# Kernel tuning notes

Measured on AMD Instinct MI355X. Metric: run time of the kernel, lower is better.

The kernel has to match this reference:

```python
import jax, jax.numpy as jnp
import numpy as np

N_NODES = 100000
N_HEDGES = 25000
N_EDGES = 1000000
NUM_GRAPHS = 64
H = 64


def _seg_mean(vals, idx, num_segments):
    s = jax.ops.segment_sum(vals, idx, num_segments=num_segments)
    cnt = jax.ops.segment_sum(jnp.ones((vals.shape[0],), vals.dtype), idx, num_segments=num_segments)
    return s / jnp.maximum(cnt, 1.0)[:, None]


def _sage(x_src, x_dst, src, dst, Wl, bl, Wr):
    # gather src features per edge, scatter-mean to dst, then lin_l(agg)+lin_r(x_dst)
    agg = _seg_mean(x_src[src], dst, x_dst.shape[0])
    return agg @ Wl + bl + x_dst @ Wr


def setup_inputs() -> dict:
    key = jax.random.key(0)
    ks = jax.random.split(key, 32)
    d = {}
    d['node_x'] = jax.random.normal(ks[0], (N_NODES, 1), jnp.float32)
    d['edge_x'] = jax.random.normal(ks[1], (N_HEDGES, 2), jnp.float32)
    d['n2e_src'] = jax.random.randint(ks[2], (N_EDGES,), 0, N_NODES)
    d['n2e_dst'] = jax.random.randint(ks[3], (N_EDGES,), 0, N_HEDGES)
    d['e2n_src'] = jax.random.randint(ks[4], (N_EDGES,), 0, N_HEDGES)
    d['e2n_dst'] = jax.random.randint(ks[5], (N_EDGES,), 0, N_NODES)
    d['node_batch'] = jnp.sort(jax.random.randint(ks[6], (N_NODES,), 0, NUM_GRAPHS))
    d['edge_batch'] = jnp.sort(jax.random.randint(ks[7], (N_HEDGES,), 0, NUM_GRAPHS))
    def w(k, shape, fan_in):
        return jax.random.normal(k, shape, jnp.float32) / np.sqrt(fan_in)
    d['Wn'] = w(ks[8], (1, H), 1); d['bn'] = jnp.zeros((H,), jnp.float32)
    d['We'] = w(ks[9], (2, H), 2); d['be'] = jnp.zeros((H,), jnp.float32)
    names = ['1l_n2e', '1r_n2e', '1l_e2n', '1r_e2n', '2l_n2e', '2r_n2e', '2l_e2n', '2r_e2n']
    for i, nm in enumerate(names):
        d['W' + nm] = w(ks[10 + i], (H, H), H)
        if 'l' in nm.split('_')[0]:
            d['b' + nm] = jnp.zeros((H,), jnp.float32)
    d['Wout'] = w(ks[20], (2 * H, 32), 2 * H)
    d['bout'] = jnp.zeros((32,), jnp.float32)
    return d


def reference(node_x, edge_x, n2e_src, n2e_dst, e2n_src, e2n_dst, node_batch, edge_batch,
              Wn, bn, We, be,
              W1l_n2e, b1l_n2e, W1r_n2e, W1l_e2n, b1l_e2n, W1r_e2n,
              W2l_n2e, b2l_n2e, W2r_n2e, W2l_e2n, b2l_e2n, W2r_e2n,
              Wout, bout):
    xn = jax.nn.relu(node_x @ Wn + bn)      # [N, H]
    xe = jax.nn.relu(edge_x @ We + be)      # [E_h, H]
    # HeteroConv layer 1 (each dst type has exactly one incoming edge type)
    xe1 = jax.nn.relu(_sage(xn, xe, n2e_src, n2e_dst, W1l_n2e, b1l_n2e, W1r_n2e))
    xn1 = jax.nn.relu(_sage(xe, xn, e2n_src, e2n_dst, W1l_e2n, b1l_e2n, W1r_e2n))
    # HeteroConv layer 2
    xe2 = jax.nn.relu(_sage(xn1, xe1, n2e_src, n2e_dst, W2l_n2e, b2l_n2e, W2r_n2e))
    xn2 = jax.nn.relu(_sage(xe1, xn1, e2n_src, e2n_dst, W2l_e2n, b2l_e2n, W2r_e2n))
    node_pool = _seg_mean(xn2, node_batch, NUM_GRAPHS)  # [G, H]
    edge_pool = _seg_mean(xe2, edge_batch, NUM_GRAPHS)  # [G, H]
    combined = jnp.concatenate([node_pool, edge_pool], axis=-1)  # [G, 2H]
    return combined @ Wout + bout  # [G, 32]
```

## Files before the change

### kernel.cpp

```cpp
#include <hip/hip_runtime.h>

#define N_NODES 100000
#define N_HEDGES 25000
#define N_EDGES 1000000
#define NG 64
#define HD 64

#define EB_SH 8
#define EB_NB 98
#define EB_CAP 12000
#define NB_SH 9
#define NB_NB 196
#define NB_CAP 6200
#define TILE 4096
#define TPS 245
#define ENC_F4 ((N_NODES + N_HEDGES) * 16)

typedef __attribute__((ext_vector_type(4))) float f4;
typedef __attribute__((ext_vector_type(4))) unsigned short us4;
typedef __attribute__((ext_vector_type(8))) unsigned short us8;
typedef __attribute__((ext_vector_type(8))) short s8b;

__device__ __forceinline__ unsigned short f2bf(float f) {
    unsigned int u = __float_as_uint(f);
    unsigned int r = (u + 0x7FFFu + ((u >> 16) & 1u)) >> 16;
    return (unsigned short)r;
}
__device__ __forceinline__ float bf2f(unsigned short h) {
    return __uint_as_float((unsigned int)h << 16);
}
__device__ __forceinline__ us4 f4_to_bf4(f4 v) {
    us4 h;
    h[0] = f2bf(v[0]); h[1] = f2bf(v[1]); h[2] = f2bf(v[2]); h[3] = f2bf(v[3]);
    return h;
}

__global__ __launch_bounds__(256) void prep(
    const float* __restrict__ W1lE, const float* __restrict__ W1rE,
    const float* __restrict__ W1lN, const float* __restrict__ W1rN,
    const float* __restrict__ W2lE, const float* __restrict__ W2rE,
    const float* __restrict__ W2lN, const float* __restrict__ W2rN,
    unsigned short* __restrict__ WtH, int* __restrict__ zbase, int zn) {
    int b = blockIdx.x, t = threadIdx.x;
    if (b < 4) {
        const float *Wl, *Wr;
        switch (b) {
            case 0: Wl = W1lE; Wr = W1rE; break;
            case 1: Wl = W1lN; Wr = W1rN; break;
            case 2: Wl = W2lE; Wr = W2rE; break;
            default: Wl = W2lN; Wr = W2rN; break;
        }
        unsigned short* o = WtH + b * 8192;
        for (int idx = t; idx < 8192; idx += 256) {
            int c = idx >> 7, k = idx & 127;
            float v = (k < 64) ? Wl[k * 64 + c] : Wr[(k - 64) * 64 + c];
            o[c * 128 + k] = f2bf(v);
        }
    } else {
        int i = (b - 4) * 256 + t;
        if (i < zn) zbase[i] = 0;
    }
}

__global__ __launch_bounds__(256) void bin_encode(
    const int* __restrict__ n2e_src, const int* __restrict__ n2e_dst,
    const int* __restrict__ e2n_src, const int* __restrict__ e2n_dst,
    int* __restrict__ binE, int* __restrict__ binN,
    int* __restrict__ gcntE, int* __restrict__ gcntN,
    const float* __restrict__ node_x, const float* __restrict__ edge_x,
    const float* __restrict__ Wn, const float* __restrict__ bn,
    const float* __restrict__ We, const float* __restrict__ be,
    unsigned short* __restrict__ xnH, unsigned short* __restrict__ xeH) {
    __shared__ int pairsL[TILE];
    __shared__ int hist[256], scanv[256], start[256], curs[256], gbase[256];
    int t = threadIdx.x;
    if ((int)blockIdx.x >= 2 * TPS) {
        int i4 = ((int)blockIdx.x - 2 * TPS) * 256 + t;
        if (i4 < N_NODES * 16) {
            int row = i4 >> 4, fq = i4 & 15;
            f4 wn = *(const f4*)(Wn + fq * 4);
            f4 bnv = *(const f4*)(bn + fq * 4);
            float xv = node_x[row];
            f4 v;
#pragma unroll
            for (int c = 0; c < 4; c++) v[c] = fmaxf(xv * wn[c] + bnv[c], 0.f);
            *(us4*)(xnH + (long)i4 * 4) = f4_to_bf4(v);
        } else if (i4 < ENC_F4) {
            int j = i4 - N_NODES * 16;
            int row = j >> 4, fq = j & 15;
            f4 w0 = *(const f4*)(We + fq * 4);
            f4 w1 = *(const f4*)(We + HD + fq * 4);
            f4 bev = *(const f4*)(be + fq * 4);
            float x0 = edge_x[2 * row], x1 = edge_x[2 * row + 1];
            f4 v;
#pragma unroll
            for (int c = 0; c < 4; c++) v[c] = fmaxf(x0 * w0[c] + x1 * w1[c] + bev[c], 0.f);
            *(us4*)(xeH + (long)j * 4) = f4_to_bf4(v);
        }
        return;
    }
    int side = (int)blockIdx.x >= TPS;
    int lb = blockIdx.x - (side ? TPS : 0);
    const int* dsts = side ? e2n_dst : n2e_dst;
    const int* srcs = side ? e2n_src : n2e_src;
    int NB = side ? NB_NB : EB_NB;
    int SH = side ? NB_SH : EB_SH;
    int CAP = side ? NB_CAP : EB_CAP;
    int* bins = side ? binN : binE;
    int* gcnt = side ? gcntN : gcntE;
    int base = lb * TILE;

    hist[t] = 0;
    __syncthreads();

    int pair[16], buck[16];
#pragma unroll
    for (int k = 0; k < 16; k++) {
        int e = base + k * 256 + t;
        if (e < N_EDGES) {
            int d = dsts[e];
            int s = srcs[e];
            buck[k] = d >> SH;
            pair[k] = ((d & ((1 << SH) - 1)) << 17) | s;
            atomicAdd(&hist[buck[k]], 1);
        } else buck[k] = -1;
    }
    __syncthreads();
    int v = hist[t];
    scanv[t] = v;
    __syncthreads();
    for (int o = 1; o < 256; o <<= 1) {
        int x = (t >= o) ? scanv[t - o] : 0;
        __syncthreads();
        scanv[t] += x;
        __syncthreads();
    }
    start[t] = scanv[t] - v;
    curs[t] = scanv[t] - v;
    if (t < NB && v > 0) gbase[t] = t * CAP + atomicAdd(&gcnt[t], v);
    __syncthreads();
    int total = scanv[255];
#pragma unroll
    for (int k = 0; k < 16; k++) {
        if (buck[k] >= 0) {
            int slot = atomicAdd(&curs[buck[k]], 1);
            pairsL[slot] = pair[k];
        }
    }
    __syncthreads();
    for (int i = t; i < total; i += 256) {
        int lo = 0, hi = NB - 1;
        while (lo < hi) { int mid = (lo + hi + 1) >> 1; if (start[mid] <= i) lo = mid; else hi = mid - 1; }
        bins[gbase[lo] + (i - start[lo])] = pairsL[i];
    }
}

__global__ __launch_bounds__(512) void fine_fill(
    const int* __restrict__ binE, const int* __restrict__ binN,
    const int* __restrict__ gcntE, const int* __restrict__ gcntN,
    int* __restrict__ off, int* __restrict__ deg,
    int* __restrict__ srtE, int* __restrict__ srtN) {
    __shared__ int hist[512], scanv[512];
    int t = threadIdx.x;
    int side = (int)blockIdx.x >= EB_NB;
    int b = blockIdx.x - (side ? EB_NB : 0);
    int NROWS = side ? 512 : 256;
    int CAP = side ? NB_CAP : EB_CAP;
    const int* bins = (side ? binN : binE) + (long)b * CAP;
    int* srt = (side ? srtN : srtE) + (long)b * CAP;
    int cnt_b = (side ? gcntN : gcntE)[b];
    int rowbase = side ? (N_HEDGES + b * 512) : b * 256;
    int nrows = (side ? N_NODES : N_HEDGES) - (side ? b * 512 : b * 256);
    if (nrows > NROWS) nrows = NROWS;

    hist[t] = 0;
    __syncthreads();
    for (int i = t; i < cnt_b; i += 512) atomicAdd(&hist[bins[i] >> 17], 1);
    __syncthreads();
    int v = hist[t];
    scanv[t] = v;
    __syncthreads();
    for (int o = 1; o < 512; o <<= 1) {
        int x = (t >= o) ? scanv[t - o] : 0;
        __syncthreads();
        scanv[t] += x;
        __syncthreads();
    }
    int excl = scanv[t] - v;
    if (t < nrows) { off[rowbase + t] = b * CAP + excl; deg[rowbase + t] = v; }
    scanv[t] = excl;
    __syncthreads();
    for (int i = t; i < cnt_b; i += 512) {
        int p = bins[i];
        int pos = atomicAdd(&scanv[p >> 17], 1);
        srt[pos] = p & 0x1FFFF;
    }
}

__global__ __launch_bounds__(256) void gather_layer(
    const unsigned short* __restrict__ xnH, const unsigned short* __restrict__ xeH,
    const int* __restrict__ off, const int* __restrict__ deg,
    const int* __restrict__ srtE, const int* __restrict__ srtN,
    unsigned short* __restrict__ aggEH, unsigned short* __restrict__ aggNH) {
    int lane = threadIdx.x & 63;
    int w = blockIdx.x * 4 + (threadIdx.x >> 6);
    int NW = gridDim.x * 4;
    int esub = lane >> 4;
    int fq = lane & 15;
    const int RT = N_HEDGES + N_NODES;
    for (int r = w; r < RT; r += NW) {
        const unsigned short* xsrc; const int* srt; unsigned short* agg; int rr, idx;
        if (r < N_HEDGES) {
            rr = r; idx = rr;
            xsrc = xnH; srt = srtE; agg = aggEH;
        } else {
            rr = r - N_HEDGES; idx = N_HEDGES + rr;
            xsrc = xeH; srt = srtN; agg = aggNH;
        }
        int lo = off[idx];
        int dg = deg[idx];
        f4 a0 = {0.f, 0.f, 0.f, 0.f}, a1 = a0;
        for (int j0 = 0; j0 < dg; j0 += 64) {
            int chunk = dg - j0;
            if (chunk > 64) chunk = 64;
            int idv = (j0 + lane < dg) ? srt[lo + j0 + lane] : 0;
            int jj = 0;
            for (; jj + 8 <= chunk; jj += 8) {
                int s0 = __shfl(idv, jj + esub);
                int s1 = __shfl(idv, jj + 4 + esub);
                us4 h0 = ((const us4*)(xsrc + (long)s0 * HD))[fq];
                us4 h1 = ((const us4*)(xsrc + (long)s1 * HD))[fq];
#pragma unroll
                for (int c = 0; c < 4; c++) { a0[c] += bf2f(h0[c]); a1[c] += bf2f(h1[c]); }
            }
            for (; jj < chunk; jj += 4) {
                int e = jj + esub;
                int s = __shfl(idv, e & 63);
                us4 h = ((const us4*)(xsrc + (long)s * HD))[fq];
                if (e < chunk) {
#pragma unroll
                    for (int c = 0; c < 4; c++) a0[c] += bf2f(h[c]);
                }
            }
        }
        f4 acc = a0 + a1;
#pragma unroll
        for (int c = 0; c < 4; c++) {
            acc[c] += __shfl_xor(acc[c], 16);
            acc[c] += __shfl_xor(acc[c], 32);
        }
        if (lane < 16) {
            float invd = 1.f / (float)(dg > 1 ? dg : 1);
            *(us4*)(agg + (long)rr * HD + fq * 4) = f4_to_bf4(acc * invd);
        }
    }
}

__global__ __launch_bounds__(256) void combine_mfma(
    const unsigned short* __restrict__ aggEH, const unsigned short* __restrict__ xeH,
    const unsigned short* __restrict__ aggNH, const unsigned short* __restrict__ xnH,
    const unsigned short* __restrict__ WtE, const float* __restrict__ blE,
    const unsigned short* __restrict__ WtN, const float* __restrict__ blN,
    unsigned short* __restrict__ outEH, unsigned short* __restrict__ outNH, int gbE) {
    __shared__ unsigned short sA[64][136];
    __shared__ unsigned short sW[64][136];
    int t = threadIdx.x;
    const unsigned short *aggH, *xdstH, *Wt;
    const float* bl;
    unsigned short* outH;
    int rows, row0;
    if ((int)blockIdx.x < gbE) {
        aggH = aggEH; xdstH = xeH; Wt = WtE; bl = blE; outH = outEH;
        rows = N_HEDGES; row0 = blockIdx.x * 64;
    } else {
        aggH = aggNH; xdstH = xnH; Wt = WtN; bl = blN; outH = outNH;
        rows = N_NODES; row0 = (blockIdx.x - gbE) * 64;
    }

#pragma unroll
    for (int q = 0; q < 4; q++) {
        int idx = q * 256 + t;
        int c = idx >> 4, ch = idx & 15;
        *(us8*)&sW[c][ch * 8] = *(const us8*)(Wt + c * 128 + ch * 8);
    }
#pragma unroll
    for (int q = 0; q < 4; q++) {
        int idx = q * 256 + t;
        int r = idx >> 4, ch = idx & 15;
        int gr = row0 + r;
        us8 v;
        if (gr < rows) {
            v = (ch < 8) ? *(const us8*)(aggH + (long)gr * HD + ch * 8)
                         : *(const us8*)(xdstH + (long)gr * HD + (ch - 8) * 8);
        } else {
            v = (us8){0, 0, 0, 0, 0, 0, 0, 0};
        }
        *(us8*)&sA[r][ch * 8] = v;
    }
    __syncthreads();

    int lane = t & 63, w = t >> 6;
    int m0 = w * 16;
    int l15 = lane & 15, quad = lane >> 4;
    f4 acc[4];
#pragma unroll
    for (int ct = 0; ct < 4; ct++) {
        float b = bl[ct * 16 + l15];
        acc[ct] = (f4){b, b, b, b};
    }
#pragma unroll
    for (int kb = 0; kb < 4; kb++) {
        s8b a = *(const s8b*)&sA[m0 + l15][kb * 32 + quad * 8];
#pragma unroll
        for (int ct = 0; ct < 4; ct++) {
            s8b bfr = *(const s8b*)&sW[ct * 16 + l15][kb * 32 + quad * 8];
            acc[ct] = __builtin_amdgcn_mfma_f32_16x16x32_bf16(a, bfr, acc[ct], 0, 0, 0);
        }
    }
#pragma unroll
    for (int ct = 0; ct < 4; ct++) {
#pragma unroll
        for (int r = 0; r < 4; r++) {
            int gr = row0 + m0 + quad * 4 + r;
            if (gr < rows) outH[(long)gr * HD + ct * 16 + l15] = f2bf(fmaxf(acc[ct][r], 0.f));
        }
    }
}

__device__ __forceinline__ int lower_bound_dev(const int* arr, int n, int key) {
    int lo = 0, hi = n;
    while (lo < hi) { int mid = (lo + hi) >> 1; if (arr[mid] < key) lo = mid + 1; else hi = mid; }
    return lo;
}

#define PB_N 8
#define PB_E 2
__global__ __launch_bounds__(256) void pool_bf(
    const unsigned short* __restrict__ xnH, const unsigned short* __restrict__ xeH,
    const int* __restrict__ node_batch, const int* __restrict__ edge_batch,
    float* __restrict__ poolN, float* __restrict__ poolE) {
    __shared__ float sp[4][64];
    int b = blockIdx.x;
    const unsigned short* x; const int* batch; float* pool; int n, g, part, P;
    if (b < NG * PB_N) { x = xnH; batch = node_batch; pool = poolN; n = N_NODES; g = b / PB_N; part = b % PB_N; P = PB_N; }
    else { b -= NG * PB_N; x = xeH; batch = edge_batch; pool = poolE; n = N_HEDGES; g = b / PB_E; part = b % PB_E; P = PB_E; }
    int s = lower_bound_dev(batch, n, g);
    int e = lower_bound_dev(batch, n, g + 1);
    int len = e - s;
    int start = s + (int)(((long)len * part) / P);
    int end = s + (int)(((long)len * (part + 1)) / P);
    int lane = threadIdx.x & 63, w = threadIdx.x >> 6;
    int fq = lane & 7, sub = lane >> 3;
    f4 a0 = {0.f, 0.f, 0.f, 0.f}, a1 = a0;
    for (int r = start + w * 8 + sub; r < end; r += 32) {
        us8 h = *(const us8*)(x + (long)r * HD + fq * 8);
#pragma unroll
        for (int c = 0; c < 4; c++) { a0[c] += bf2f(h[c]); a1[c] += bf2f(h[c + 4]); }
    }
#pragma unroll
    for (int c = 0; c < 4; c++) {
        a0[c] += __shfl_xor(a0[c], 8);  a1[c] += __shfl_xor(a1[c], 8);
        a0[c] += __shfl_xor(a0[c], 16); a1[c] += __shfl_xor(a1[c], 16);
        a0[c] += __shfl_xor(a0[c], 32); a1[c] += __shfl_xor(a1[c], 32);
    }
    if (lane < 8) {
        *(f4*)&sp[w][fq * 8] = a0;
        *(f4*)&sp[w][fq * 8 + 4] = a1;
    }
    __syncthreads();
    if (threadIdx.x < 64) {
        int tt = threadIdx.x;
        float v = sp[0][tt] + sp[1][tt] + sp[2][tt] + sp[3][tt];
        if (v != 0.f) atomicAdd(&pool[g * HD + tt], v);
    }
}

__global__ __launch_bounds__(64) void final_readout(
    const float* __restrict__ poolN, const float* __restrict__ poolE,
    const int* __restrict__ node_batch, const int* __restrict__ edge_batch,
    const float* __restrict__ Wout, const float* __restrict__ bout,
    float* __restrict__ out) {
    __shared__ float inv[2];
    int g = blockIdx.x, t = threadIdx.x;
    if (t < 2) {
        const int* arr = t ? edge_batch : node_batch;
        int n = t ? N_HEDGES : N_NODES;
        int lo = lower_bound_dev(arr, n, g);
        int hi = lower_bound_dev(arr, n, g + 1);
        int c = hi - lo;
        inv[t] = 1.f / (float)(c > 1 ? c : 1);
    }
    __syncthreads();
    if (t < 32) {
        float iN = inv[0], iE = inv[1];
        float s = bout[t];
#pragma unroll 8
        for (int k = 0; k < HD; k++)
            s += poolN[g * HD + k] * iN * Wout[k * 32 + t]
               + poolE[g * HD + k] * iE * Wout[(HD + k) * 32 + t];
        out[g * 32 + t] = s;
    }
}

extern "C" void kernel_launch(void* const* d_in, const int* in_sizes, int n_in,
                              void* d_out, int out_size, void* d_ws, size_t ws_size,
                              hipStream_t stream) {
    const float* node_x = (const float*)d_in[0];
    const float* edge_x = (const float*)d_in[1];
    const int* n2e_src = (const int*)d_in[2];
    const int* n2e_dst = (const int*)d_in[3];
    const int* e2n_src = (const int*)d_in[4];
    const int* e2n_dst = (const int*)d_in[5];
    const int* node_batch = (const int*)d_in[6];
    const int* edge_batch = (const int*)d_in[7];
    const float* Wn = (const float*)d_in[8];
    const float* bn = (const float*)d_in[9];
    const float* We = (const float*)d_in[10];
    const float* be = (const float*)d_in[11];
    const float* W1l_n2e = (const float*)d_in[12];
    const float* b1l_n2e = (const float*)d_in[13];
    const float* W1r_n2e = (const float*)d_in[14];
    const float* W1l_e2n = (const float*)d_in[15];
    const float* b1l_e2n = (const float*)d_in[16];
    const float* W1r_e2n = (const float*)d_in[17];
    const float* W2l_n2e = (const float*)d_in[18];
    const float* b2l_n2e = (const float*)d_in[19];
    const float* W2r_n2e = (const float*)d_in[20];
    const float* W2l_e2n = (const float*)d_in[21];
    const float* b2l_e2n = (const float*)d_in[22];
    const float* W2r_e2n = (const float*)d_in[23];
    const float* Wout = (const float*)d_in[24];
    const float* bout = (const float*)d_in[25];
    float* out = (float*)d_out;

    unsigned short* AH0 = (unsigned short*)d_ws;
    unsigned short* BH0 = AH0 + N_NODES * HD;
    unsigned short* AH1 = BH0 + N_HEDGES * HD;
    unsigned short* BH1 = AH1 + N_NODES * HD;
    unsigned short* aggNH = BH1 + N_HEDGES * HD;
    unsigned short* aggEH = aggNH + N_NODES * HD;
    unsigned short* WtH = aggEH + N_HEDGES * HD;
    float* poolN = (float*)(WtH + 4 * 8192);
    float* poolE = poolN + NG * HD;
    int* gcntE = (int*)(poolE + NG * HD);
    int* gcntN = gcntE + EB_NB;
    int* off = gcntN + NB_NB;
    int* deg = off + (N_HEDGES + N_NODES);
    int* binE = deg + (N_HEDGES + N_NODES);
    int* binN = binE + EB_NB * EB_CAP;
    int* srtE = binN + NB_NB * NB_CAP;
    int* srtN = srtE + EB_NB * EB_CAP;

    const int Bt = 256;

    int zn = 2 * NG * HD + EB_NB + NB_NB;
    prep<<<4 + (zn + Bt - 1) / Bt, Bt, 0, stream>>>(
        W1l_n2e, W1r_n2e, W1l_e2n, W1r_e2n,
        W2l_n2e, W2r_n2e, W2l_e2n, W2r_e2n,
        WtH, (int*)poolN, zn);

    int encBlocks = (ENC_F4 + Bt - 1) / Bt;
    bin_encode<<<2 * TPS + encBlocks, Bt, 0, stream>>>(
        n2e_src, n2e_dst, e2n_src, e2n_dst, binE, binN, gcntE, gcntN,
        node_x, edge_x, Wn, bn, We, be, AH0, BH0);

    fine_fill<<<EB_NB + NB_NB, 512, 0, stream>>>(binE, binN, gcntE, gcntN,
                                                 off, deg, srtE, srtN);

    int gbE = (N_HEDGES + 63) / 64;
    int gbN = (N_NODES + 63) / 64;
    int gridC = gbE + gbN;

    gather_layer<<<2048, Bt, 0, stream>>>(AH0, BH0, off, deg, srtE, srtN, aggEH, aggNH);
    combine_mfma<<<gridC, Bt, 0, stream>>>(aggEH, BH0, aggNH, AH0,
                                           WtH, b1l_n2e, WtH + 8192, b1l_e2n,
                                           BH1, AH1, gbE);

    gather_layer<<<2048, Bt, 0, stream>>>(AH1, BH1, off, deg, srtE, srtN, aggEH, aggNH);
    combine_mfma<<<gridC, Bt, 0, stream>>>(aggEH, BH1, aggNH, AH1,
                                           WtH + 16384, b2l_n2e, WtH + 24576, b2l_e2n,
                                           BH0, AH0, gbE);

    pool_bf<<<NG * PB_N + NG * PB_E, Bt, 0, stream>>>(AH0, BH0, node_batch, edge_batch, poolN, poolE);

    final_readout<<<NG, 64, 0, stream>>>(poolN, poolE, node_batch, edge_batch, Wout, bout, out);
}
```

Before: 189.0 us.

## Store features in chunk-major layout and gather per 8-feature chunk

Feature tensors move from row-major [rows][64] bf16 to a chunk-major [8][rows][8] layout. The gather kernel becomes gather_cm: each block handles one 8-feature chunk and each group of 8 lanes reduces one destination row. The aim is to shrink each chunk's gather working set, about 1.6 MB for the 100000-node source, so random source reads hit cache more often. Node-side sorted indices shrink to 16-bit. Encoder, combine, and pool kernels are updated to read and write the new layout. In exchange, the index list is reread by all 8 chunk blocks, and combine's scattered per-element bf16 stores become strided.

```diff
diff --git a/kernel.cpp b/kernel.cpp
--- a/kernel.cpp
+++ b/kernel.cpp
@@ -70,32 +70,34 @@
     const float* __restrict__ node_x, const float* __restrict__ edge_x,
     const float* __restrict__ Wn, const float* __restrict__ bn,
     const float* __restrict__ We, const float* __restrict__ be,
-    unsigned short* __restrict__ xnH, unsigned short* __restrict__ xeH) {
+    unsigned short* __restrict__ xnC, unsigned short* __restrict__ xeC) {
     __shared__ int pairsL[TILE];
     __shared__ int hist[256], scanv[256], start[256], curs[256], gbase[256];
     int t = threadIdx.x;
     if ((int)blockIdx.x >= 2 * TPS) {
         int i4 = ((int)blockIdx.x - 2 * TPS) * 256 + t;
         if (i4 < N_NODES * 16) {
-            int row = i4 >> 4, fq = i4 & 15;
-            f4 wn = *(const f4*)(Wn + fq * 4);
-            f4 bnv = *(const f4*)(bn + fq * 4);
+            int row = i4 >> 4, q = i4 & 15;
+            int cc = q >> 1, hh = (q & 1) * 4;
+            f4 wn = *(const f4*)(Wn + cc * 8 + hh);
+            f4 bnv = *(const f4*)(bn + cc * 8 + hh);
             float xv = node_x[row];
             f4 v;
 #pragma unroll
             for (int c = 0; c < 4; c++) v[c] = fmaxf(xv * wn[c] + bnv[c], 0.f);
-            *(us4*)(xnH + (long)i4 * 4) = f4_to_bf4(v);
+            *(us4*)(xnC + ((long)cc * N_NODES + row) * 8 + hh) = f4_to_bf4(v);
         } else if (i4 < ENC_F4) {
             int j = i4 - N_NODES * 16;
-            int row = j >> 4, fq = j & 15;
-            f4 w0 = *(const f4*)(We + fq * 4);
-            f4 w1 = *(const f4*)(We + HD + fq * 4);
-            f4 bev = *(const f4*)(be + fq * 4);
+            int row = j >> 4, q = j & 15;
+            int cc = q >> 1, hh = (q & 1) * 4;
+            f4 w0 = *(const f4*)(We + cc * 8 + hh);
+            f4 w1 = *(const f4*)(We + HD + cc * 8 + hh);
+            f4 bev = *(const f4*)(be + cc * 8 + hh);
             float x0 = edge_x[2 * row], x1 = edge_x[2 * row + 1];
             f4 v;
 #pragma unroll
             for (int c = 0; c < 4; c++) v[c] = fmaxf(x0 * w0[c] + x1 * w1[c] + bev[c], 0.f);
-            *(us4*)(xeH + (long)j * 4) = f4_to_bf4(v);
+            *(us4*)(xeC + ((long)cc * N_HEDGES + row) * 8 + hh) = f4_to_bf4(v);
         }
         return;
     }
@@ -159,7 +161,7 @@
     const int* __restrict__ binE, const int* __restrict__ binN,
     const int* __restrict__ gcntE, const int* __restrict__ gcntN,
     int* __restrict__ off, int* __restrict__ deg,
-    int* __restrict__ srtE, int* __restrict__ srtN) {
+    int* __restrict__ srtE, unsigned short* __restrict__ srtN) {
     __shared__ int hist[512], scanv[512];
     int t = threadIdx.x;
     int side = (int)blockIdx.x >= EB_NB;
@@ -167,11 +169,12 @@
     int NROWS = side ? 512 : 256;
     int CAP = side ? NB_CAP : EB_CAP;
     const int* bins = (side ? binN : binE) + (long)b * CAP;
-    int* srt = (side ? srtN : srtE) + (long)b * CAP;
     int cnt_b = (side ? gcntN : gcntE)[b];
     int rowbase = side ? (N_HEDGES + b * 512) : b * 256;
     int nrows = (side ? N_NODES : N_HEDGES) - (side ? b * 512 : b * 256);
     if (nrows > NROWS) nrows = NROWS;
+    int* srtEb = srtE + (long)b * CAP;
+    unsigned short* srtNb = srtN + (long)b * CAP;
 
     hist[t] = 0;
     __syncthreads();
@@ -193,95 +196,118 @@
     for (int i = t; i < cnt_b; i += 512) {
         int p = bins[i];
         int pos = atomicAdd(&scanv[p >> 17], 1);
-        srt[pos] = p & 0x1FFFF;
-    }
-}
-
-__global__ __launch_bounds__(256) void gather_layer(
-    const unsigned short* __restrict__ xnH, const unsigned short* __restrict__ xeH,
+        if (side) srtNb[pos] = (unsigned short)(p & 0x1FFFF);
+        else srtEb[pos] = p & 0x1FFFF;
+    }
+}
+
+__global__ __launch_bounds__(256) void gather_cm(
+    const unsigned short* __restrict__ xnC, const unsigned short* __restrict__ xeC,
     const int* __restrict__ off, const int* __restrict__ deg,
-    const int* __restrict__ srtE, const int* __restrict__ srtN,
-    unsigned short* __restrict__ aggEH, unsigned short* __restrict__ aggNH) {
-    int lane = threadIdx.x & 63;
-    int w = blockIdx.x * 4 + (threadIdx.x >> 6);
-    int NW = gridDim.x * 4;
-    int esub = lane >> 4;
-    int fq = lane & 15;
-    const int RT = N_HEDGES + N_NODES;
-    for (int r = w; r < RT; r += NW) {
-        const unsigned short* xsrc; const int* srt; unsigned short* agg; int rr, idx;
-        if (r < N_HEDGES) {
-            rr = r; idx = rr;
-            xsrc = xnH; srt = srtE; agg = aggEH;
-        } else {
-            rr = r - N_HEDGES; idx = N_HEDGES + rr;
-            xsrc = xeH; srt = srtN; agg = aggNH;
-        }
-        int lo = off[idx];
-        int dg = deg[idx];
-        f4 a0 = {0.f, 0.f, 0.f, 0.f}, a1 = a0;
-        for (int j0 = 0; j0 < dg; j0 += 64) {
-            int chunk = dg - j0;
-            if (chunk > 64) chunk = 64;
-            int idv = (j0 + lane < dg) ? srt[lo + j0 + lane] : 0;
-            int jj = 0;
-            for (; jj + 8 <= chunk; jj += 8) {
-                int s0 = __shfl(idv, jj + esub);
-                int s1 = __shfl(idv, jj + 4 + esub);
-                us4 h0 = ((const us4*)(xsrc + (long)s0 * HD))[fq];
-                us4 h1 = ((const us4*)(xsrc + (long)s1 * HD))[fq];
-#pragma unroll
-                for (int c = 0; c < 4; c++) { a0[c] += bf2f(h0[c]); a1[c] += bf2f(h1[c]); }
-            }
-            for (; jj < chunk; jj += 4) {
-                int e = jj + esub;
-                int s = __shfl(idv, e & 63);
-                us4 h = ((const us4*)(xsrc + (long)s * HD))[fq];
-                if (e < chunk) {
-#pragma unroll
-                    for (int c = 0; c < 4; c++) a0[c] += bf2f(h[c]);
+    const int* __restrict__ srtE, const unsigned short* __restrict__ srtN,
+    unsigned short* __restrict__ aggEC, unsigned short* __restrict__ aggNC) {
+    int t = threadIdx.x;
+    int lane = t & 63, w = t >> 6;
+    int c = blockIdx.x & 7;
+    int bg = blockIdx.x >> 3;
+    int NBG = gridDim.x >> 3;
+    int sub = lane & 7;
+    int rg = lane >> 3;
+    const int EG = N_HEDGES / 8;
+    const int NGRP = (N_HEDGES + N_NODES) / 8;
+    const unsigned short* srcN = xnC + (long)c * (N_NODES * 8);
+    const unsigned short* srcE = xeC + (long)c * (N_HEDGES * 8);
+
+    for (int g0 = bg * 4 + w; g0 < NGRP; g0 += NBG * 4) {
+        int r = g0 * 8 + rg;
+        int lo = off[r], dg = deg[r];
+        f4 a0 = {0.f, 0.f, 0.f, 0.f}, a1 = a0, b0 = a0, b1 = a0;
+        if (g0 < EG) {
+            int j = sub;
+            for (; j + 8 < dg; j += 16) {
+                int s0 = srtE[lo + j];
+                int s1 = srtE[lo + j + 8];
+                us8 h0 = *(const us8*)(srcN + (long)s0 * 8);
+                us8 h1 = *(const us8*)(srcN + (long)s1 * 8);
+#pragma unroll
+                for (int i = 0; i < 4; i++) {
+                    a0[i] += bf2f(h0[i]); a1[i] += bf2f(h0[i + 4]);
+                    b0[i] += bf2f(h1[i]); b1[i] += bf2f(h1[i + 4]);
                 }
             }
-        }
-        f4 acc = a0 + a1;
-#pragma unroll
-        for (int c = 0; c < 4; c++) {
-            acc[c] += __shfl_xor(acc[c], 16);
-            acc[c] += __shfl_xor(acc[c], 32);
-        }
-        if (lane < 16) {
+            if (j < dg) {
+                int s = srtE[lo + j];
+                us8 h = *(const us8*)(srcN + (long)s * 8);
+#pragma unroll
+                for (int i = 0; i < 4; i++) { a0[i] += bf2f(h[i]); a1[i] += bf2f(h[i + 4]); }
+            }
+        } else {
+            int j = sub;
+            for (; j + 8 < dg; j += 16) {
+                int s0 = srtN[lo + j];
+                int s1 = srtN[lo + j + 8];
+                us8 h0 = *(const us8*)(srcE + (long)s0 * 8);
+                us8 h1 = *(const us8*)(srcE + (long)s1 * 8);
+#pragma unroll
+                for (int i = 0; i < 4; i++) {
+                    a0[i] += bf2f(h0[i]); a1[i] += bf2f(h0[i + 4]);
+                    b0[i] += bf2f(h1[i]); b1[i] += bf2f(h1[i + 4]);
+                }
+            }
+            if (j < dg) {
+                int s = srtN[lo + j];
+                us8 h = *(const us8*)(srcE + (long)s * 8);
+#pragma unroll
+                for (int i = 0; i < 4; i++) { a0[i] += bf2f(h[i]); a1[i] += bf2f(h[i + 4]); }
+            }
+        }
+        a0 += b0; a1 += b1;
+#pragma unroll
+        for (int m = 1; m <= 4; m <<= 1) {
+#pragma unroll
+            for (int i = 0; i < 4; i++) {
+                a0[i] += __shfl_xor(a0[i], m);
+                a1[i] += __shfl_xor(a1[i], m);
+            }
+        }
+        if (sub == 0) {
             float invd = 1.f / (float)(dg > 1 ? dg : 1);
-            *(us4*)(agg + (long)rr * HD + fq * 4) = f4_to_bf4(acc * invd);
+            us8 o;
+            us4 p0 = f4_to_bf4(a0 * invd), p1 = f4_to_bf4(a1 * invd);
+#pragma unroll
+            for (int i = 0; i < 4; i++) { o[i] = p0[i]; o[i + 4] = p1[i]; }
+            if (g0 < EG) *(us8*)(aggEC + ((long)c * N_HEDGES + r) * 8) = o;
+            else *(us8*)(aggNC + ((long)c * N_NODES + (r - N_HEDGES)) * 8) = o;
         }
     }
 }
 
 __global__ __launch_bounds__(256) void combine_mfma(
-    const unsigned short* __restrict__ aggEH, const unsigned short* __restrict__ xeH,
-    const unsigned short* __restrict__ aggNH, const unsigned short* __restrict__ xnH,
+    const unsigned short* __restrict__ aggEC, const unsigned short* __restrict__ xeC,
+    const unsigned short* __restrict__ aggNC, const unsigned short* __restrict__ xnC,
     const unsigned short* __restrict__ WtE, const float* __restrict__ blE,
     const unsigned short* __restrict__ WtN, const float* __restrict__ blN,
-    unsigned short* __restrict__ outEH, unsigned short* __restrict__ outNH, int gbE) {
+    unsigned short* __restrict__ outEC, unsigned short* __restrict__ outNC, int gbE) {
     __shared__ unsigned short sA[64][136];
     __shared__ unsigned short sW[64][136];
     int t = threadIdx.x;
-    const unsigned short *aggH, *xdstH, *Wt;
+    const unsigned short *aggC, *xdstC, *Wt;
     const float* bl;
-    unsigned short* outH;
+    unsigned short* outC;
     int rows, row0;
     if ((int)blockIdx.x < gbE) {
-        aggH = aggEH; xdstH = xeH; Wt = WtE; bl = blE; outH = outEH;
+        aggC = aggEC; xdstC = xeC; Wt = WtE; bl = blE; outC = outEC;
         rows = N_HEDGES; row0 = blockIdx.x * 64;
     } else {
-        aggH = aggNH; xdstH = xnH; Wt = WtN; bl = blN; outH = outNH;
+        aggC = aggNC; xdstC = xnC; Wt = WtN; bl = blN; outC = outNC;
         rows = N_NODES; row0 = (blockIdx.x - gbE) * 64;
     }
 
 #pragma unroll
     for (int q = 0; q < 4; q++) {
         int idx = q * 256 + t;
-        int c = idx >> 4, ch = idx & 15;
-        *(us8*)&sW[c][ch * 8] = *(const us8*)(Wt + c * 128 + ch * 8);
+        int cw = idx >> 4, ch = idx & 15;
+        *(us8*)&sW[cw][ch * 8] = *(const us8*)(Wt + cw * 128 + ch * 8);
     }
 #pragma unroll
     for (int q = 0; q < 4; q++) {
@@ -290,8 +316,8 @@
         int gr = row0 + r;
         us8 v;
         if (gr < rows) {
-            v = (ch < 8) ? *(const us8*)(aggH + (long)gr * HD + ch * 8)
-                         : *(const us8*)(xdstH + (long)gr * HD + (ch - 8) * 8);
+            v = (ch < 8) ? *(const us8*)(aggC + ((long)ch * rows + gr) * 8)
+                         : *(const us8*)(xdstC + ((long)(ch - 8) * rows + gr) * 8);
         } else {
             v = (us8){0, 0, 0, 0, 0, 0, 0, 0};
         }
@@ -322,7 +348,10 @@
 #pragma unroll
         for (int r = 0; r < 4; r++) {
             int gr = row0 + m0 + quad * 4 + r;
-            if (gr < rows) outH[(long)gr * HD + ct * 16 + l15] = f2bf(fmaxf(acc[ct][r], 0.f));
+            if (gr < rows) {
+                int col = ct * 16 + l15;
+                outC[((long)(col >> 3) * rows + gr) * 8 + (col & 7)] = f2bf(fmaxf(acc[ct][r], 0.f));
+            }
         }
     }
 }
@@ -336,36 +365,39 @@
 #define PB_N 8
 #define PB_E 2
 __global__ __launch_bounds__(256) void pool_bf(
-    const unsigned short* __restrict__ xnH, const unsigned short* __restrict__ xeH,
+    const unsigned short* __restrict__ xnC, const unsigned short* __restrict__ xeC,
     const int* __restrict__ node_batch, const int* __restrict__ edge_batch,
     float* __restrict__ poolN, float* __restrict__ poolE) {
     __shared__ float sp[4][64];
     int b = blockIdx.x;
     const unsigned short* x; const int* batch; float* pool; int n, g, part, P;
-    if (b < NG * PB_N) { x = xnH; batch = node_batch; pool = poolN; n = N_NODES; g = b / PB_N; part = b % PB_N; P = PB_N; }
-    else { b -= NG * PB_N; x = xeH; batch = edge_batch; pool = poolE; n = N_HEDGES; g = b / PB_E; part = b % PB_E; P = PB_E; }
+    if (b < NG * PB_N) { x = xnC; batch = node_batch; pool = poolN; n = N_NODES; g = b / PB_N; part = b % PB_N; P = PB_N; }
+    else { b -= NG * PB_N; x = xeC; batch = edge_batch; pool = poolE; n = N_HEDGES; g = b / PB_E; part = b % PB_E; P = PB_E; }
     int s = lower_bound_dev(batch, n, g);
     int e = lower_bound_dev(batch, n, g + 1);
     int len = e - s;
     int start = s + (int)(((long)len * part) / P);
     int end = s + (int)(((long)len * (part + 1)) / P);
     int lane = threadIdx.x & 63, w = threadIdx.x >> 6;
-    int fq = lane & 7, sub = lane >> 3;
+    int cc = lane & 7, rw = lane >> 3;
+    const unsigned short* xc = x + (long)cc * n * 8;
     f4 a0 = {0.f, 0.f, 0.f, 0.f}, a1 = a0;
-    for (int r = start + w * 8 + sub; r < end; r += 32) {
-        us8 h = *(const us8*)(x + (long)r * HD + fq * 8);
-#pragma unroll
-        for (int c = 0; c < 4; c++) { a0[c] += bf2f(h[c]); a1[c] += bf2f(h[c + 4]); }
-    }
-#pragma unroll
-    for (int c = 0; c < 4; c++) {
-        a0[c] += __shfl_xor(a0[c], 8);  a1[c] += __shfl_xor(a1[c], 8);
-        a0[c] += __shfl_xor(a0[c], 16); a1[c] += __shfl_xor(a1[c], 16);
-        a0[c] += __shfl_xor(a0[c], 32); a1[c] += __shfl_xor(a1[c], 32);
-    }
-    if (lane < 8) {
-        *(f4*)&sp[w][fq * 8] = a0;
-        *(f4*)&sp[w][fq * 8 + 4] = a1;
+    for (int r = start + w * 8 + rw; r < end; r += 32) {
+        us8 h = *(const us8*)(xc + (long)r * 8);
+#pragma unroll
+        for (int i = 0; i < 4; i++) { a0[i] += bf2f(h[i]); a1[i] += bf2f(h[i + 4]); }
+    }
+#pragma unroll
+    for (int m = 8; m <= 32; m <<= 1) {
+#pragma unroll
+        for (int i = 0; i < 4; i++) {
+            a0[i] += __shfl_xor(a0[i], m);
+            a1[i] += __shfl_xor(a1[i], m);
+        }
+    }
+    if (rw == 0) {
+        *(f4*)&sp[w][cc * 8] = a0;
+        *(f4*)&sp[w][cc * 8 + 4] = a1;
     }
     __syncthreads();
     if (threadIdx.x < 64) {
@@ -433,13 +465,13 @@
     const float* bout = (const float*)d_in[25];
     float* out = (float*)d_out;
 
-    unsigned short* AH0 = (unsigned short*)d_ws;
-    unsigned short* BH0 = AH0 + N_NODES * HD;
-    unsigned short* AH1 = BH0 + N_HEDGES * HD;
-    unsigned short* BH1 = AH1 + N_NODES * HD;
-    unsigned short* aggNH = BH1 + N_HEDGES * HD;
-    unsigned short* aggEH = aggNH + N_NODES * HD;
-    unsigned short* WtH = aggEH + N_HEDGES * HD;
+    unsigned short* xnC0 = (unsigned short*)d_ws;
+    unsigned short* xeC0 = xnC0 + N_NODES * HD;
+    unsigned short* xnC1 = xeC0 + N_HEDGES * HD;
+    unsigned short* xeC1 = xnC1 + N_NODES * HD;
+    unsigned short* aggNC = xeC1 + N_HEDGES * HD;
+    unsigned short* aggEC = aggNC + N_NODES * HD;
+    unsigned short* WtH = aggEC + N_HEDGES * HD;
     float* poolN = (float*)(WtH + 4 * 8192);
     float* poolE = poolN + NG * HD;
     int* gcntE = (int*)(poolE + NG * HD);
@@ -449,7 +481,7 @@
     int* binE = deg + (N_HEDGES + N_NODES);
     int* binN = binE + EB_NB * EB_CAP;
     int* srtE = binN + NB_NB * NB_CAP;
-    int* srtN = srtE + EB_NB * EB_CAP;
+    unsigned short* srtN = (unsigned short*)(srtE + EB_NB * EB_CAP);
 
     const int Bt = 256;
 
@@ -462,7 +494,7 @@
     int encBlocks = (ENC_F4 + Bt - 1) / Bt;
     bin_encode<<<2 * TPS + encBlocks, Bt, 0, stream>>>(
         n2e_src, n2e_dst, e2n_src, e2n_dst, binE, binN, gcntE, gcntN,
-        node_x, edge_x, Wn, bn, We, be, AH0, BH0);
+        node_x, edge_x, Wn, bn, We, be, xnC0, xeC0);
 
     fine_fill<<<EB_NB + NB_NB, 512, 0, stream>>>(binE, binN, gcntE, gcntN,
                                                  off, deg, srtE, srtN);
@@ -471,17 +503,17 @@
     int gbN = (N_NODES + 63) / 64;
     int gridC = gbE + gbN;
 
-    gather_layer<<<2048, Bt, 0, stream>>>(AH0, BH0, off, deg, srtE, srtN, aggEH, aggNH);
-    combine_mfma<<<gridC, Bt, 0, stream>>>(aggEH, BH0, aggNH, AH0,
+    gather_cm<<<2048, Bt, 0, stream>>>(xnC0, xeC0, off, deg, srtE, srtN, aggEC, aggNC);
+    combine_mfma<<<gridC, Bt, 0, stream>>>(aggEC, xeC0, aggNC, xnC0,
                                            WtH, b1l_n2e, WtH + 8192, b1l_e2n,
-                                           BH1, AH1, gbE);
-
-    gather_layer<<<2048, Bt, 0, stream>>>(AH1, BH1, off, deg, srtE, srtN, aggEH, aggNH);
-    combine_mfma<<<gridC, Bt, 0, stream>>>(aggEH, BH1, aggNH, AH1,
+                                           xeC1, xnC1, gbE);
+
+    gather_cm<<<2048, Bt, 0, stream>>>(xnC1, xeC1, off, deg, srtE, srtN, aggEC, aggNC);
+    combine_mfma<<<gridC, Bt, 0, stream>>>(aggEC, xeC1, aggNC, xnC1,
                                            WtH + 16384, b2l_n2e, WtH + 24576, b2l_e2n,
-                                           BH0, AH0, gbE);
-
-    pool_bf<<<NG * PB_N + NG * PB_E, Bt, 0, stream>>>(AH0, BH0, node_batch, edge_batch, poolN, poolE);
+                                           xeC0, xnC0, gbE);
+
+    pool_bf<<<NG * PB_N + NG * PB_E, Bt, 0, stream>>>(xnC0, xeC0, node_batch, edge_batch, poolN, poolE);
 
     final_readout<<<NG, 64, 0, stream>>>(poolN, poolE, node_batch, edge_batch, Wout, bout, out);
 }
```

New measurement: 262.7 us. 1.39x slower.

## Fuse neighbor gather with MFMA combine and store node-side indices as u16

Applied to the files above, without the earlier changes.

Merges the gather-mean kernel and the MFMA linear-combine kernel into one kernel per layer. Each block aggregates its 64 destination rows into shared memory and then runs the bf16 MFMA against the concatenated weights, with the x_dst fragment loaded straight into registers. This removes the global round trip of the aggregate buffers and one launch per layer. Node-side sorted source indices (hyperedge ids below 65536) are stored as 16-bit to halve that index traffic. The trade-off is that each wave now processes a fixed 16 rows instead of grid-striding, so load balance across uneven degrees may suffer.

```diff
diff --git a/kernel.cpp b/kernel.cpp
--- a/kernel.cpp
+++ b/kernel.cpp
@@ -159,7 +159,7 @@
     const int* __restrict__ binE, const int* __restrict__ binN,
     const int* __restrict__ gcntE, const int* __restrict__ gcntN,
     int* __restrict__ off, int* __restrict__ deg,
-    int* __restrict__ srtE, int* __restrict__ srtN) {
+    int* __restrict__ srtE, unsigned short* __restrict__ srtN) {
     __shared__ int hist[512], scanv[512];
     int t = threadIdx.x;
     int side = (int)blockIdx.x >= EB_NB;
@@ -167,11 +167,12 @@
     int NROWS = side ? 512 : 256;
     int CAP = side ? NB_CAP : EB_CAP;
     const int* bins = (side ? binN : binE) + (long)b * CAP;
-    int* srt = (side ? srtN : srtE) + (long)b * CAP;
     int cnt_b = (side ? gcntN : gcntE)[b];
     int rowbase = side ? (N_HEDGES + b * 512) : b * 256;
     int nrows = (side ? N_NODES : N_HEDGES) - (side ? b * 512 : b * 256);
     if (nrows > NROWS) nrows = NROWS;
+    int* srtEb = srtE + (long)b * CAP;
+    unsigned short* srtNb = srtN + (long)b * CAP;
 
     hist[t] = 0;
     __syncthreads();
@@ -193,37 +194,69 @@
     for (int i = t; i < cnt_b; i += 512) {
         int p = bins[i];
         int pos = atomicAdd(&scanv[p >> 17], 1);
-        srt[pos] = p & 0x1FFFF;
-    }
-}
-
-__global__ __launch_bounds__(256) void gather_layer(
+        if (side) srtNb[pos] = (unsigned short)(p & 0x1FFFF);
+        else srtEb[pos] = p & 0x1FFFF;
+    }
+}
+
+__global__ __launch_bounds__(256) void sage_fused(
     const unsigned short* __restrict__ xnH, const unsigned short* __restrict__ xeH,
     const int* __restrict__ off, const int* __restrict__ deg,
-    const int* __restrict__ srtE, const int* __restrict__ srtN,
-    unsigned short* __restrict__ aggEH, unsigned short* __restrict__ aggNH) {
-    int lane = threadIdx.x & 63;
-    int w = blockIdx.x * 4 + (threadIdx.x >> 6);
-    int NW = gridDim.x * 4;
+    const int* __restrict__ srtE, const unsigned short* __restrict__ srtN,
+    const unsigned short* __restrict__ WtE, const float* __restrict__ blE,
+    const unsigned short* __restrict__ WtN, const float* __restrict__ blN,
+    unsigned short* __restrict__ outEH, unsigned short* __restrict__ outNH, int gbE) {
+    __shared__ unsigned short sA[64][72];
+    __shared__ unsigned short sW[64][136];
+    int t = threadIdx.x;
+    int lane = t & 63, wv = t >> 6;
+    bool eSide = (int)blockIdx.x < gbE;
+    const unsigned short* xsrc = eSide ? xnH : xeH;
+    const unsigned short* xdstH = eSide ? xeH : xnH;
+    const unsigned short* Wt = eSide ? WtE : WtN;
+    const float* bl = eSide ? blE : blN;
+    unsigned short* outH = eSide ? outEH : outNH;
+    int rows = eSide ? N_HEDGES : N_NODES;
+    int row0 = (eSide ? (int)blockIdx.x : (int)blockIdx.x - gbE) * 64;
+    int rbase = eSide ? 0 : N_HEDGES;
+
+    int m0 = wv * 16;
+    int l15 = lane & 15, quad = lane >> 4;
+
+    s8b xf[2];
+    {
+        int grf = row0 + m0 + l15;
+#pragma unroll
+        for (int kb2 = 0; kb2 < 2; kb2++) {
+            if (grf < rows)
+                xf[kb2] = *(const s8b*)(xdstH + (long)grf * HD + kb2 * 32 + quad * 8);
+            else
+                xf[kb2] = (s8b){0, 0, 0, 0, 0, 0, 0, 0};
+        }
+    }
+
+#pragma unroll
+    for (int q = 0; q < 4; q++) {
+        int idx = q * 256 + t;
+        int c = idx >> 4, ch = idx & 15;
+        *(us8*)&sW[c][ch * 8] = *(const us8*)(Wt + c * 128 + ch * 8);
+    }
+
     int esub = lane >> 4;
     int fq = lane & 15;
-    const int RT = N_HEDGES + N_NODES;
-    for (int r = w; r < RT; r += NW) {
-        const unsigned short* xsrc; const int* srt; unsigned short* agg; int rr, idx;
-        if (r < N_HEDGES) {
-            rr = r; idx = rr;
-            xsrc = xnH; srt = srtE; agg = aggEH;
-        } else {
-            rr = r - N_HEDGES; idx = N_HEDGES + rr;
-            xsrc = xeH; srt = srtN; agg = aggNH;
-        }
-        int lo = off[idx];
-        int dg = deg[idx];
+    for (int i = 0; i < 16; i++) {
+        int rr = wv * 16 + i;
+        int gr = row0 + rr;
+        if (gr >= rows) break;
+        int lo = off[rbase + gr];
+        int dg = deg[rbase + gr];
         f4 a0 = {0.f, 0.f, 0.f, 0.f}, a1 = a0;
         for (int j0 = 0; j0 < dg; j0 += 64) {
             int chunk = dg - j0;
             if (chunk > 64) chunk = 64;
-            int idv = (j0 + lane < dg) ? srt[lo + j0 + lane] : 0;
+            int idv;
+            if (eSide) idv = (j0 + lane < dg) ? srtE[lo + j0 + lane] : 0;
+            else idv = (j0 + lane < dg) ? (int)srtN[lo + j0 + lane] : 0;
             int jj = 0;
             for (; jj + 8 <= chunk; jj += 8) {
                 int s0 = __shfl(idv, jj + esub);
@@ -251,57 +284,11 @@
         }
         if (lane < 16) {
             float invd = 1.f / (float)(dg > 1 ? dg : 1);
-            *(us4*)(agg + (long)rr * HD + fq * 4) = f4_to_bf4(acc * invd);
-        }
-    }
-}
-
-__global__ __launch_bounds__(256) void combine_mfma(
-    const unsigned short* __restrict__ aggEH, const unsigned short* __restrict__ xeH,
-    const unsigned short* __restrict__ aggNH, const unsigned short* __restrict__ xnH,
-    const unsigned short* __restrict__ WtE, const float* __restrict__ blE,
-    const unsigned short* __restrict__ WtN, const float* __restrict__ blN,
-    unsigned short* __restrict__ outEH, unsigned short* __restrict__ outNH, int gbE) {
-    __shared__ unsigned short sA[64][136];
-    __shared__ unsigned short sW[64][136];
-    int t = threadIdx.x;
-    const unsigned short *aggH, *xdstH, *Wt;
-    const float* bl;
-    unsigned short* outH;
-    int rows, row0;
-    if ((int)blockIdx.x < gbE) {
-        aggH = aggEH; xdstH = xeH; Wt = WtE; bl = blE; outH = outEH;
-        rows = N_HEDGES; row0 = blockIdx.x * 64;
-    } else {
-        aggH = aggNH; xdstH = xnH; Wt = WtN; bl = blN; outH = outNH;
-        rows = N_NODES; row0 = (blockIdx.x - gbE) * 64;
-    }
-
-#pragma unroll
-    for (int q = 0; q < 4; q++) {
-        int idx = q * 256 + t;
-        int c = idx >> 4, ch = idx & 15;
-        *(us8*)&sW[c][ch * 8] = *(const us8*)(Wt + c * 128 + ch * 8);
-    }
-#pragma unroll
-    for (int q = 0; q < 4; q++) {
-        int idx = q * 256 + t;
-        int r = idx >> 4, ch = idx & 15;
-        int gr = row0 + r;
-        us8 v;
-        if (gr < rows) {
-            v = (ch < 8) ? *(const us8*)(aggH + (long)gr * HD + ch * 8)
-                         : *(const us8*)(xdstH + (long)gr * HD + (ch - 8) * 8);
-        } else {
-            v = (us8){0, 0, 0, 0, 0, 0, 0, 0};
-        }
-        *(us8*)&sA[r][ch * 8] = v;
-    }
-    __syncthreads();
-
-    int lane = t & 63, w = t >> 6;
-    int m0 = w * 16;
-    int l15 = lane & 15, quad = lane >> 4;
+            *(us4*)&sA[rr][fq * 4] = f4_to_bf4(acc * invd);
+        }
+    }
+    __syncthreads();
+
     f4 acc[4];
 #pragma unroll
     for (int ct = 0; ct < 4; ct++) {
@@ -310,7 +297,9 @@
     }
 #pragma unroll
     for (int kb = 0; kb < 4; kb++) {
-        s8b a = *(const s8b*)&sA[m0 + l15][kb * 32 + quad * 8];
+        s8b a;
+        if (kb < 2) a = *(const s8b*)&sA[m0 + l15][kb * 32 + quad * 8];
+        else a = xf[kb - 2];
 #pragma unroll
         for (int ct = 0; ct < 4; ct++) {
             s8b bfr = *(const s8b*)&sW[ct * 16 + l15][kb * 32 + quad * 8];
@@ -437,9 +426,7 @@
     unsigned short* BH0 = AH0 + N_NODES * HD;
     unsigned short* AH1 = BH0 + N_HEDGES * HD;
     unsigned short* BH1 = AH1 + N_NODES * HD;
-    unsigned short* aggNH = BH1 + N_HEDGES * HD;
-    unsigned short* aggEH = aggNH + N_NODES * HD;
-    unsigned short* WtH = aggEH + N_HEDGES * HD;
+    unsigned short* WtH = BH1 + N_HEDGES * HD;
     float* poolN = (float*)(WtH + 4 * 8192);
     float* poolE = poolN + NG * HD;
     int* gcntE = (int*)(poolE + NG * HD);
@@ -449,7 +436,7 @@
     int* binE = deg + (N_HEDGES + N_NODES);
     int* binN = binE + EB_NB * EB_CAP;
     int* srtE = binN + NB_NB * NB_CAP;
-    int* srtN = srtE + EB_NB * EB_CAP;
+    unsigned short* srtN = (unsigned short*)(srtE + EB_NB * EB_CAP);
 
     const int Bt = 256;
 
@@ -471,15 +458,13 @@
     int gbN = (N_NODES + 63) / 64;
     int gridC = gbE + gbN;
 
-    gather_layer<<<2048, Bt, 0, stream>>>(AH0, BH0, off, deg, srtE, srtN, aggEH, aggNH);
-    combine_mfma<<<gridC, Bt, 0, stream>>>(aggEH, BH0, aggNH, AH0,
-                                           WtH, b1l_n2e, WtH + 8192, b1l_e2n,
-                                           BH1, AH1, gbE);
-
-    gather_layer<<<2048, Bt, 0, stream>>>(AH1, BH1, off, deg, srtE, srtN, aggEH, aggNH);
-    combine_mfma<<<gridC, Bt, 0, stream>>>(aggEH, BH1, aggNH, AH1,
-                                           WtH + 16384, b2l_n2e, WtH + 24576, b2l_e2n,
-                                           BH0, AH0, gbE);
+    sage_fused<<<gridC, Bt, 0, stream>>>(AH0, BH0, off, deg, srtE, srtN,
+                                         WtH, b1l_n2e, WtH + 8192, b1l_e2n,
+                                         BH1, AH1, gbE);
+
+    sage_fused<<<gridC, Bt, 0, stream>>>(AH1, BH1, off, deg, srtE, srtN,
+                                         WtH + 16384, b2l_n2e, WtH + 24576, b2l_e2n,
+                                         BH0, AH0, gbE);
 
     pool_bf<<<NG * PB_N + NG * PB_E, Bt, 0, stream>>>(AH0, BH0, node_batch, edge_batch, poolN, poolE);
 
```

New measurement: 223.5 us. 1.18x slower.
